# Kernel tuning notes

Hardware: AMD Instinct MI355X
Metric: run time of the kernel (lower is better)

## Reference

```python
import jax, jax.numpy as jnp
import numpy as np
import math

D = 768
H = 12
DK = D // H
DI = 3072
EPS_LN = 1e-12
NEG = -1e9


def layernorm(x, g, b):
    mu = jnp.mean(x, axis=-1, keepdims=True)
    var = jnp.mean(jnp.square(x - mu), axis=-1, keepdims=True)
    return (x - mu) * jax.lax.rsqrt(var + EPS_LN) * g + b


def setup_inputs() -> dict:
    key = jax.random.key(0)
    ks = jax.random.split(key, 16)
    B, S = 16, 512
    sd = 0.02
    inp = {
        "hidden_states": jax.random.normal(ks[0], (B, S, D), dtype=jnp.float32),
        "constituent_prior": jnp.zeros((B, S, S), dtype=jnp.float32),
        "attention_mask": jnp.ones((B, S), dtype=jnp.int32),
        # MultiHeadedAttention: 4 linears (q, k, v, out)
        "Wq": jax.random.normal(ks[1], (D, D)) * sd, "bq": jnp.zeros((D,)),
        "Wk": jax.random.normal(ks[2], (D, D)) * sd, "bk": jnp.zeros((D,)),
        "Wv": jax.random.normal(ks[3], (D, D)) * sd, "bv": jnp.zeros((D,)),
        "Wo": jax.random.normal(ks[4], (D, D)) * sd, "bo": jnp.zeros((D,)),
        # GroupAttention: key/query linears + LayerNorm
        "gWk": jax.random.normal(ks[5], (D, D)) * sd, "gbk": jnp.zeros((D,)),
        "gWq": jax.random.normal(ks[6], (D, D)) * sd, "gbq": jnp.zeros((D,)),
        "g_ln_g": jnp.ones((D,)), "g_ln_b": jnp.zeros((D,)),
        # BertIntermediate / BertOutput
        "Wi": jax.random.normal(ks[7], (D, DI)) * sd, "bi": jnp.zeros((DI,)),
        "Wout": jax.random.normal(ks[8], (DI, D)) * sd, "bout": jnp.zeros((D,)),
        "ln_g": jnp.ones((D,)), "ln_b": jnp.zeros((D,)),
    }
    return {k: v.astype(jnp.float32) if v.dtype == jnp.float32 or jnp.issubdtype(v.dtype, jnp.floating) else v for k, v in inp.items()}


def group_attention(x, attention_mask, prior, gWk, gbk, gWq, gbq, g_ln_g, g_ln_b):
    B, S, _ = x.shape
    a = jnp.eye(S, k=1, dtype=jnp.float32)      # super-diagonal
    c = jnp.eye(S, k=-1, dtype=jnp.float32)     # sub-diagonal
    eye = jnp.eye(S, dtype=jnp.float32)
    tri = jnp.triu(jnp.ones((S, S), dtype=jnp.float32))  # upper-tri incl. diag

    h = layernorm(x, g_ln_g, g_ln_b)
    k = h @ gWk + gbk
    q = h @ gWq + gbq
    scores = jnp.einsum("bsd,btd->bst", q, k) / D
    # mask[b,i,j] = attention_mask[b,j] & (a+c)[i,j]  (only +/-1 neighbors)
    mask = attention_mask.astype(jnp.float32)[:, None, :] * (a + c)[None]
    scores = jnp.where(mask == 0, NEG, scores)
    neigh = jax.nn.softmax(scores, axis=-1)
    neigh = jnp.sqrt(neigh * jnp.swapaxes(neigh, -2, -1) + 1e-9)
    neigh = prior + (1.0 - prior) * neigh

    # prefix log-sums along the super-diagonal via triangular matmuls
    t = jnp.where(a[None] == 0, 0.0, jnp.log(neigh + 1e-9)) @ tri
    C = jnp.exp(jnp.einsum("ij,bjk->bik", tri, t))
    C = jnp.where((tri - eye)[None] == 0, 0.0, C)   # keep strictly upper tri
    C = C + jnp.swapaxes(C, -2, -1) + jnp.where(eye[None] == 0, 1e-9, neigh)
    return C, neigh


def multi_head_attention(x, group_prob, attention_mask, Wq, bq, Wk, bk, Wv, bv, Wo, bo):
    B, S, _ = x.shape
    def split(y):  # [B,S,D] -> [B,H,S,DK]
        return y.reshape(B, S, H, DK).transpose(0, 2, 1, 3)
    q = split(x @ Wq + bq)
    k = split(x @ Wk + bk)
    v = split(x @ Wv + bv)
    scores = jnp.einsum("bhsd,bhtd->bhst", q, k) / math.sqrt(DK)
    eye = jnp.eye(S, dtype=jnp.int32)
    # combined mask: allow key j if attention_mask[b,j] or j == i (diagonal)
    cm = (attention_mask[:, None, None, :] | eye[None, None]) != 0
    scores = jnp.where(cm, scores, NEG)
    p = jax.nn.softmax(scores, axis=-1) * group_prob[:, None]  # [B,H,S,S]
    out = jnp.einsum("bhst,bhtd->bhsd", p, v)
    out = out.transpose(0, 2, 1, 3).reshape(B, S, D)
    return out @ Wo + bo


def reference(hidden_states, constituent_prior, attention_mask,
              Wq, bq, Wk, bk, Wv, bv, Wo, bo,
              gWk, gbk, gWq, gbq, g_ln_g, g_ln_b,
              Wi, bi, Wout, bout, ln_g, ln_b):
    C, neigh = group_attention(hidden_states, attention_mask, constituent_prior,
                               gWk, gbk, gWq, gbq, g_ln_g, g_ln_b)
    attn_out = multi_head_attention(hidden_states, C, attention_mask,
                                    Wq, bq, Wk, bk, Wv, bv, Wo, bo)
    inter = jax.nn.gelu(attn_out @ Wi + bi, approximate=False)
    layer_out = layernorm(inter @ Wout + bout + attn_out, ln_g, ln_b)
    return (layer_out, C, neigh, attn_out)
```

## Files before the change

### kernel.cpp

```cpp
#include <hip/hip_runtime.h>
#include <math.h>

typedef unsigned short ushort_t;
typedef __attribute__((ext_vector_type(8))) short bf16x8;
typedef __attribute__((ext_vector_type(4))) float f32x4;

#define Dt 768
#define Mrows 8192

__device__ __forceinline__ ushort_t f2b(float f) {
    union { float f; unsigned int u; } v; v.f = f;
    unsigned int u = v.u;
    unsigned int r = (u + 0x7fffu + ((u >> 16) & 1u)) >> 16;
    return (ushort_t)r;
}
__device__ __forceinline__ float b2f(ushort_t u) {
    union { unsigned int u; float f; } v; v.u = ((unsigned int)u) << 16;
    return v.f;
}
__device__ __forceinline__ f32x4 mfma16(bf16x8 a, bf16x8 b, f32x4 c) {
    return __builtin_amdgcn_mfma_f32_16x16x32_bf16(a, b, c, 0, 0, 0);
}
__device__ __forceinline__ float gelu_exact(float v) {
    return 0.5f * v * (1.0f + erff(v * 0.70710678118654752f));
}
__device__ __forceinline__ void gl2lds16(const ushort_t* g, ushort_t* l) {
    __builtin_amdgcn_global_load_lds((const __attribute__((address_space(1))) void*)g,
                                     (__attribute__((address_space(3))) void*)l,
                                     16, 0, 0);
}

__global__ __launch_bounds__(256)
void tconv6_kernel(const float* i0, const float* i1, const float* i2,
                   const float* i3, const float* i4, const float* i5,
                   ushort_t* o0, ushort_t* o1, ushort_t* o2,
                   ushort_t* o3, ushort_t* o4, ushort_t* o5)
{
    const float* in; ushort_t* out;
    switch (blockIdx.z) {
        case 0: in = i0; out = o0; break;
        case 1: in = i1; out = o1; break;
        case 2: in = i2; out = o2; break;
        case 3: in = i3; out = o3; break;
        case 4: in = i4; out = o4; break;
        default: in = i5; out = o5; break;
    }
    __shared__ float T[32][33];
    int t = threadIdx.x;
    int n0 = blockIdx.x * 32, k0 = blockIdx.y * 32;
    int r = t >> 3, c4 = (t & 7) * 4;
    float4 v = *(const float4*)(in + (size_t)(k0 + r) * 768 + n0 + c4);
    T[r][c4] = v.x; T[r][c4 + 1] = v.y; T[r][c4 + 2] = v.z; T[r][c4 + 3] = v.w;
    __syncthreads();
    int nl = t >> 3, k4 = (t & 7) * 4;
    unsigned int lo = (unsigned int)f2b(T[k4][nl]) | ((unsigned int)f2b(T[k4 + 1][nl]) << 16);
    unsigned int hi = (unsigned int)f2b(T[k4 + 2][nl]) | ((unsigned int)f2b(T[k4 + 3][nl]) << 16);
    uint2 o; o.x = lo; o.y = hi;
    *(uint2*)(out + (size_t)(n0 + nl) * 768 + k0 + k4) = o;
}

__global__ __launch_bounds__(256)
void tconv_kernel(const float* __restrict__ in, ushort_t* __restrict__ out,
                  int K, int N)
{
    __shared__ float T[32][33];
    int t = threadIdx.x;
    int n0 = blockIdx.x * 32, k0 = blockIdx.y * 32;
    int r = t >> 3, c4 = (t & 7) * 4;
    float4 v = *(const float4*)(in + (size_t)(k0 + r) * N + n0 + c4);
    T[r][c4] = v.x; T[r][c4 + 1] = v.y; T[r][c4 + 2] = v.z; T[r][c4 + 3] = v.w;
    __syncthreads();
    int nl = t >> 3, k4 = (t & 7) * 4;
    unsigned int lo = (unsigned int)f2b(T[k4][nl]) | ((unsigned int)f2b(T[k4 + 1][nl]) << 16);
    unsigned int hi = (unsigned int)f2b(T[k4 + 2][nl]) | ((unsigned int)f2b(T[k4 + 3][nl]) << 16);
    uint2 o; o.x = lo; o.y = hi;
    *(uint2*)(out + (size_t)(n0 + nl) * K + k0 + k4) = o;
}

__global__ __launch_bounds__(256)
void bconcat_kernel(const float* bq, const float* bk, const float* bv,
                    const float* gbq, const float* gbk,
                    float* bqkv, float* gbqk)
{
    int g = blockIdx.x * 256 + threadIdx.x;
    if (g < 768)       bqkv[g] = bq[g];
    else if (g < 1536) bqkv[g] = bk[g - 768];
    else if (g < 2304) bqkv[g] = bv[g - 1536];
    else if (g < 3072) gbqk[g - 2304] = gbq[g - 2304];
    else if (g < 3840) gbqk[g - 2304] = gbk[g - 3072];
}

__global__ __launch_bounds__(256)
void lnx_kernel(const float* __restrict__ x, const float* __restrict__ g,
                const float* __restrict__ be, ushort_t* __restrict__ xb,
                ushort_t* __restrict__ hb)
{
    int row = blockIdx.x;
    const float* xr = x + (size_t)row * Dt;
    int t = threadIdx.x;
    float v0 = xr[t], v1 = xr[t + 256], v2 = xr[t + 512];
    ushort_t* xrow = xb + (size_t)row * Dt;
    xrow[t] = f2b(v0); xrow[t + 256] = f2b(v1); xrow[t + 512] = f2b(v2);
    float s = v0 + v1 + v2;
    #pragma unroll
    for (int off = 32; off; off >>= 1) s += __shfl_xor(s, off, 64);
    __shared__ float r1[4], r2[4];
    if ((t & 63) == 0) r1[t >> 6] = s;
    __syncthreads();
    float mu = (r1[0] + r1[1] + r1[2] + r1[3]) * (1.0f / Dt);
    float d0 = v0 - mu, d1 = v1 - mu, d2 = v2 - mu;
    float sq = d0 * d0 + d1 * d1 + d2 * d2;
    #pragma unroll
    for (int off = 32; off; off >>= 1) sq += __shfl_xor(sq, off, 64);
    if ((t & 63) == 0) r2[t >> 6] = sq;
    __syncthreads();
    float var = (r2[0] + r2[1] + r2[2] + r2[3]) * (1.0f / Dt);
    float rs = 1.0f / sqrtf(var + 1e-12f);
    ushort_t* hrow = hb + (size_t)row * Dt;
    hrow[t]       = f2b(d0 * rs * g[t]       + be[t]);
    hrow[t + 256] = f2b(d1 * rs * g[t + 256] + be[t + 256]);
    hrow[t + 512] = f2b(d2 * rs * g[t + 512] + be[t + 512]);
}

__global__ __launch_bounds__(256)
void ln_kernel(const float* __restrict__ x, const float* __restrict__ g,
               const float* __restrict__ be, float* __restrict__ out)
{
    int row = blockIdx.x;
    const float* xr = x + (size_t)row * Dt;
    int t = threadIdx.x;
    float v0 = xr[t], v1 = xr[t + 256], v2 = xr[t + 512];
    float s = v0 + v1 + v2;
    #pragma unroll
    for (int off = 32; off; off >>= 1) s += __shfl_xor(s, off, 64);
    __shared__ float r1[4], r2[4];
    if ((t & 63) == 0) r1[t >> 6] = s;
    __syncthreads();
    float mu = (r1[0] + r1[1] + r1[2] + r1[3]) * (1.0f / Dt);
    float d0 = v0 - mu, d1 = v1 - mu, d2 = v2 - mu;
    float sq = d0 * d0 + d1 * d1 + d2 * d2;
    #pragma unroll
    for (int off = 32; off; off >>= 1) sq += __shfl_xor(sq, off, 64);
    if ((t & 63) == 0) r2[t >> 6] = sq;
    __syncthreads();
    float var = (r2[0] + r2[1] + r2[2] + r2[3]) * (1.0f / Dt);
    float rs = 1.0f / sqrtf(var + 1e-12f);
    float* orow = out + (size_t)row * Dt;
    orow[t]       = d0 * rs * g[t]       + be[t];
    orow[t + 256] = d1 * rs * g[t + 256] + be[t + 256];
    orow[t + 512] = d2 * rs * g[t + 512] + be[t + 512];
}

enum { EPI_BF16 = 1, EPI_QKV = 2, EPI_DUAL = 3, EPI_GELU = 4, EPI_RES = 5, EPI_ACC = 6 };

template<int BN, int EPI>
__global__ __launch_bounds__(256)
void gemm128(const ushort_t* __restrict__ A, const ushort_t* __restrict__ Bt,
             const float* __restrict__ bias, const float* __restrict__ res,
             float* __restrict__ Cf, ushort_t* __restrict__ O0,
             ushort_t* __restrict__ O1, ushort_t* __restrict__ O2,
             int K, int ldb, int ldc)
{
    constexpr int NF = BN / 32;
    constexpr int AHALF = 128 * 32;
    constexpr int BHALF = BN * 32;
    __shared__ ushort_t As[2 * AHALF];
    __shared__ ushort_t Bs[2 * BHALF];
    int t = threadIdx.x;
    int w = t >> 6, l = t & 63;
    int wr = w >> 1, wc = w & 1;
    int lr = l & 15, lg = l >> 4;

    int nwg = gridDim.x * gridDim.y;
    int bid = blockIdx.y * gridDim.x + blockIdx.x;
    int per = nwg >> 3;
    int sw  = (bid & 7) * per + (bid >> 3);
    int bn = (sw % gridDim.x) * BN;
    int bm = (sw / gridDim.x) * 128;

    const ushort_t* gA0 = A + (size_t)(bm + (t >> 2)) * K + ((t & 3) << 3);
    const ushort_t* gA1 = A + (size_t)(bm + 64 + (t >> 2)) * K + ((t & 3) << 3);
    const ushort_t* gB0 = Bt + (size_t)(bn + (t >> 2)) * ldb + ((t & 3) << 3);
    const ushort_t* gB1 = (BN == 128) ?
        Bt + (size_t)(bn + 64 + (t >> 2)) * ldb + ((t & 3) << 3) : nullptr;
    int woff = (w << 9);

    f32x4 acc[4][NF];
    #pragma unroll
    for (int m = 0; m < 4; ++m)
        #pragma unroll
        for (int n = 0; n < NF; ++n) acc[m][n] = (f32x4)0.0f;

    gl2lds16(gA0, As + woff);
    gl2lds16(gA1, As + 2048 + woff);
    gl2lds16(gB0, Bs + woff);
    if (BN == 128) gl2lds16(gB1, Bs + 2048 + woff);
    __syncthreads();

    int cur = 0;
    for (int k0 = 0; k0 < K; k0 += 32) {
        if (k0 + 32 < K) {
            int nb = (cur ^ 1);
            gl2lds16(gA0 + k0 + 32, As + nb * AHALF + woff);
            gl2lds16(gA1 + k0 + 32, As + nb * AHALF + 2048 + woff);
            gl2lds16(gB0 + k0 + 32, Bs + nb * BHALF + woff);
            if (BN == 128) gl2lds16(gB1 + k0 + 32, Bs + nb * BHALF + 2048 + woff);
        }
        const ushort_t* Ab = As + cur * AHALF;
        const ushort_t* Bb = Bs + cur * BHALF;
        bf16x8 af[4], bfv[NF];
        #pragma unroll
        for (int m = 0; m < 4; ++m)
            af[m] = *(const bf16x8*)&Ab[(wr * 64 + m * 16 + lr) * 32 + lg * 8];
        #pragma unroll
        for (int n = 0; n < NF; ++n)
            bfv[n] = *(const bf16x8*)&Bb[(wc * (BN / 2) + n * 16 + lr) * 32 + lg * 8];
        __builtin_amdgcn_s_setprio(1);
        #pragma unroll
        for (int m = 0; m < 4; ++m)
            #pragma unroll
            for (int n = 0; n < NF; ++n)
                acc[m][n] = mfma16(af[m], bfv[n], acc[m][n]);
        __builtin_amdgcn_s_setprio(0);
        __syncthreads();
        cur ^= 1;
    }

    #pragma unroll
    for (int m = 0; m < 4; ++m) {
        int row0 = bm + wr * 64 + m * 16 + lg * 4;
        #pragma unroll
        for (int n = 0; n < NF; ++n) {
            int ng = bn + wc * (BN / 2) + n * 16 + lr;
            float v0 = acc[m][n][0], v1 = acc[m][n][1];
            float v2 = acc[m][n][2], v3 = acc[m][n][3];
            if (EPI != EPI_ACC) {
                float bv = bias[ng];
                v0 += bv; v1 += bv; v2 += bv; v3 += bv;
            }
            if (EPI == EPI_BF16) {
                O0[(size_t)(row0 + 0) * ldc + ng] = f2b(v0);
                O0[(size_t)(row0 + 1) * ldc + ng] = f2b(v1);
                O0[(size_t)(row0 + 2) * ldc + ng] = f2b(v2);
                O0[(size_t)(row0 + 3) * ldc + ng] = f2b(v3);
            } else if (EPI == EPI_QKV) {
                if (bn < 768) {
                    O0[(size_t)(row0 + 0) * 768 + ng] = f2b(v0 * 0.125f);
                    O0[(size_t)(row0 + 1) * 768 + ng] = f2b(v1 * 0.125f);
                    O0[(size_t)(row0 + 2) * 768 + ng] = f2b(v2 * 0.125f);
                    O0[(size_t)(row0 + 3) * 768 + ng] = f2b(v3 * 0.125f);
                } else if (bn < 1536) {
                    int c = ng - 768;
                    O1[(size_t)(row0 + 0) * 768 + c] = f2b(v0);
                    O1[(size_t)(row0 + 1) * 768 + c] = f2b(v1);
                    O1[(size_t)(row0 + 2) * 768 + c] = f2b(v2);
                    O1[(size_t)(row0 + 3) * 768 + c] = f2b(v3);
                } else {
                    int dk = ng - 1536;
                    unsigned int lo = (unsigned int)f2b(v0) | ((unsigned int)f2b(v1) << 16);
                    unsigned int hi = (unsigned int)f2b(v2) | ((unsigned int)f2b(v3) << 16);
                    uint2 o; o.x = lo; o.y = hi;
                    *(uint2*)(O2 + (size_t)dk * Mrows + row0) = o;
                }
            } else if (EPI == EPI_DUAL) {
                Cf[(size_t)(row0 + 0) * ldc + ng] = v0;
                Cf[(size_t)(row0 + 1) * ldc + ng] = v1;
                Cf[(size_t)(row0 + 2) * ldc + ng] = v2;
                Cf[(size_t)(row0 + 3) * ldc + ng] = v3;
                O0[(size_t)(row0 + 0) * ldc + ng] = f2b(v0);
                O0[(size_t)(row0 + 1) * ldc + ng] = f2b(v1);
                O0[(size_t)(row0 + 2) * ldc + ng] = f2b(v2);
                O0[(size_t)(row0 + 3) * ldc + ng] = f2b(v3);
            } else if (EPI == EPI_GELU) {
                O0[(size_t)(row0 + 0) * ldc + ng] = f2b(gelu_exact(v0));
                O0[(size_t)(row0 + 1) * ldc + ng] = f2b(gelu_exact(v1));
                O0[(size_t)(row0 + 2) * ldc + ng] = f2b(gelu_exact(v2));
                O0[(size_t)(row0 + 3) * ldc + ng] = f2b(gelu_exact(v3));
            } else if (EPI == EPI_RES) {
                Cf[(size_t)(row0 + 0) * ldc + ng] = v0 + res[(size_t)(row0 + 0) * Dt + ng];
                Cf[(size_t)(row0 + 1) * ldc + ng] = v1 + res[(size_t)(row0 + 1) * Dt + ng];
                Cf[(size_t)(row0 + 2) * ldc + ng] = v2 + res[(size_t)(row0 + 2) * Dt + ng];
                Cf[(size_t)(row0 + 3) * ldc + ng] = v3 + res[(size_t)(row0 + 3) * Dt + ng];
            } else if (EPI == EPI_ACC) {
                Cf[(size_t)(row0 + 0) * ldc + ng] += v0;
                Cf[(size_t)(row0 + 1) * ldc + ng] += v1;
                Cf[(size_t)(row0 + 2) * ldc + ng] += v2;
                Cf[(size_t)(row0 + 3) * ldc + ng] += v3;
            }
        }
    }
}

__global__ __launch_bounds__(256)
void group_scores_kernel(const ushort_t* __restrict__ GQK, const int* __restrict__ am,
                         float* __restrict__ smU, float* __restrict__ smD,
                         int* __restrict__ emptyF)
{
    int gi = blockIdx.x;
    int b = gi >> 9, s = gi & 511;
    int t = threadIdx.x;
    const ushort_t* qr = GQK + (size_t)gi * 1536;
    bool hasU = (s < 511) && (am[(b << 9) + s + 1] != 0);
    bool hasD = (s > 0)   && (am[(b << 9) + s - 1] != 0);
    float su = 0.0f, sd = 0.0f;
    if (hasU) {
        const ushort_t* kr = GQK + (size_t)(gi + 1) * 1536 + 768;
        for (int c = t; c < Dt; c += 256) su += b2f(qr[c]) * b2f(kr[c]);
    }
    if (hasD) {
        const ushort_t* kr = GQK + (size_t)(gi - 1) * 1536 + 768;
        for (int c = t; c < Dt; c += 256) sd += b2f(qr[c]) * b2f(kr[c]);
    }
    #pragma unroll
    for (int off = 32; off; off >>= 1) { su += __shfl_xor(su, off, 64); sd += __shfl_xor(sd, off, 64); }
    __shared__ float rU[4], rD[4];
    if ((t & 63) == 0) { rU[t >> 6] = su; rD[t >> 6] = sd; }
    __syncthreads();
    if (t == 0) {
        su = (rU[0] + rU[1] + rU[2] + rU[3]) * (1.0f / Dt);
        sd = (rD[0] + rD[1] + rD[2] + rD[3]) * (1.0f / Dt);
        float u, d2; int emp = 0;
        if (hasU && hasD) {
            float m = fmaxf(su, sd);
            float eu = __expf(su - m), ed = __expf(sd - m);
            float inv = 1.0f / (eu + ed);
            u = eu * inv; d2 = ed * inv;
        } else if (hasU) { u = 1.0f; d2 = 0.0f; }
        else if (hasD)   { u = 0.0f; d2 = 1.0f; }
        else { u = d2 = 1.0f / 512.0f; emp = 1; }
        smU[gi] = u; smD[gi] = d2; emptyF[gi] = emp;
    }
}

__global__ __launch_bounds__(64)
void prefix_kernel(const float* __restrict__ prior, const float* __restrict__ smU,
                   const float* __restrict__ smD, float* __restrict__ P)
{
    int b = blockIdx.x;
    int l = threadIdx.x;
    float lv[8];
    float run = 0.0f;
    #pragma unroll
    for (int e = 0; e < 8; ++e) {
        int j = l * 8 + e;
        float lj = 0.0f;
        if (j < 511) {
            float pr = prior[((size_t)((b << 9) + j)) * 512 + j + 1];
            float nv = pr + (1.0f - pr) *
                       sqrtf(smU[(b << 9) + j] * smD[(b << 9) + j + 1] + 1e-9f);
            lj = logf(nv + 1e-9f);
        }
        lv[e] = run;
        run += lj;
    }
    float tot = run;
    float scan = tot;
    #pragma unroll
    for (int off = 1; off < 64; off <<= 1) {
        float n = __shfl_up(scan, off, 64);
        if (l >= off) scan += n;
    }
    float excl = scan - tot;
    #pragma unroll
    for (int e = 0; e < 8; ++e)
        P[b * 512 + l * 8 + e] = excl + lv[e];
}

__global__ __launch_bounds__(512)
void neigh_cfill_kernel(const float* __restrict__ prior,
                        const float* __restrict__ smU, const float* __restrict__ smD,
                        const int* __restrict__ emptyF, const float* __restrict__ P,
                        float* __restrict__ ne_out, float* __restrict__ C_out,
                        ushort_t* __restrict__ CB)
{
    int bi = blockIdx.x;
    int j  = threadIdx.x;
    int b = bi >> 9, i = bi & 511;
    int bj = (b << 9) + j;
    const float invS = 1.0f / 512.0f;
    float fij, fji;
    if (j == i + 1)      { fij = smU[bi]; fji = smD[bj]; }
    else if (j == i - 1) { fij = smD[bi]; fji = smU[bj]; }
    else { fij = emptyF[bi] ? invS : 0.0f; fji = emptyF[bj] ? invS : 0.0f; }
    float val = sqrtf(fij * fji + 1e-9f);
    float pr = prior[(size_t)bi * 512 + j];
    float nv = pr + (1.0f - pr) * val;
    ne_out[(size_t)bi * 512 + j] = nv;
    float pi = P[bi], pj = P[bj];
    float v;
    if (j > i)      v = expf(pj - pi) + 1e-9f;
    else if (j < i) v = expf(pi - pj) + 1e-9f;
    else            v = nv;
    C_out[(size_t)bi * 512 + j] = v;
    CB[(size_t)bi * 512 + j] = f2b(v);
}

#define SMAX 12.0f
__global__ __launch_bounds__(256)
void mha_mfma(const ushort_t* __restrict__ q, const ushort_t* __restrict__ k,
              const ushort_t* __restrict__ vt, const int* __restrict__ am,
              const ushort_t* __restrict__ CB, ushort_t* __restrict__ ctx)
{
    __shared__ ushort_t Qs[64][72];
    __shared__ ushort_t Ks[64][72];
    __shared__ ushort_t Vs[64][72];
    __shared__ ushort_t Ps[64][72];
    int t = threadIdx.x;
    int w = t >> 6, l = t & 63;
    int lr = l & 15, lg = l >> 4;
    int kb8 = lg << 3;
    int bid = (blockIdx.z * 12 + blockIdx.y) * 8 + blockIdx.x;
    int sw = (bid & 7) * 192 + (bid >> 3);
    int qt = sw & 7, h = (sw >> 3) % 12, b = sw / 96;
    int hoff = h * 64;
    int q0 = qt * 64;
    int q0g = (b << 9) + q0;
    int myrow = w * 16 + lg * 4;

    #pragma unroll
    for (int i = 0; i < 2; ++i) {
        int c = t + i * 256;
        int r = c >> 3, dc = (c & 7) << 3;
        *(uint4*)&Qs[r][dc] = *(const uint4*)(q + (size_t)(q0g + r) * Dt + hoff + dc);
    }

    f32x4 oacc[4];
    #pragma unroll
    for (int n = 0; n < 4; ++n) oacc[n] = (f32x4)0.0f;
    float l_run[4] = {0.0f, 0.0f, 0.0f, 0.0f};

    for (int kb = 0; kb < 8; ++kb) {
        __syncthreads();
        #pragma unroll
        for (int i = 0; i < 2; ++i) {
            int c = t + i * 256;
            int r = c >> 3, dc = (c & 7) << 3;
            *(uint4*)&Ks[r][dc] =
                *(const uint4*)(k + (size_t)((b << 9) + kb * 64 + r) * Dt + hoff + dc);
            *(uint4*)&Vs[r][dc] =
                *(const uint4*)(vt + (size_t)(hoff + r) * Mrows + (b << 9) + kb * 64 + dc);
        }
        __syncthreads();

        int amv[4];
        #pragma unroll
        for (int n = 0; n < 4; ++n) amv[n] = am[(b << 9) + kb * 64 + n * 16 + lr];
        float cc[4][4];
        #pragma unroll
        for (int n = 0; n < 4; ++n)
            #pragma unroll
            for (int r = 0; r < 4; ++r)
                cc[n][r] = b2f(CB[(size_t)(q0g + myrow + r) * 512 + kb * 64 + n * 16 + lr]);

        f32x4 s[4];
        #pragma unroll
        for (int n = 0; n < 4; ++n) s[n] = (f32x4)0.0f;
        __builtin_amdgcn_s_setprio(1);
        #pragma unroll
        for (int ks = 0; ks < 2; ++ks) {
            bf16x8 aq = *(const bf16x8*)&Qs[w * 16 + lr][ks * 32 + kb8];
            #pragma unroll
            for (int n = 0; n < 4; ++n) {
                bf16x8 bk = *(const bf16x8*)&Ks[n * 16 + lr][ks * 32 + kb8];
                s[n] = mfma16(aq, bk, s[n]);
            }
        }
        __builtin_amdgcn_s_setprio(0);

        float pf[4][4];
        #pragma unroll
        for (int n = 0; n < 4; ++n) {
            int key = kb * 64 + n * 16 + lr;
            #pragma unroll
            for (int r = 0; r < 4; ++r) {
                int qrow = q0 + myrow + r;
                bool ok = (amv[n] != 0) || (key == qrow);
                float p = ok ? __expf(s[n][r] - SMAX) : 0.0f;
                pf[n][r] = p;
                l_run[r] += p;
            }
        }
        #pragma unroll
        for (int n = 0; n < 4; ++n)
            #pragma unroll
            for (int r = 0; r < 4; ++r)
                Ps[myrow + r][n * 16 + lr] = f2b(pf[n][r] * cc[n][r]);

        __builtin_amdgcn_s_setprio(1);
        #pragma unroll
        for (int ks = 0; ks < 2; ++ks) {
            bf16x8 ap = *(const bf16x8*)&Ps[w * 16 + lr][ks * 32 + kb8];
            #pragma unroll
            for (int n = 0; n < 4; ++n) {
                bf16x8 bv = *(const bf16x8*)&Vs[n * 16 + lr][ks * 32 + kb8];
                oacc[n] = mfma16(ap, bv, oacc[n]);
            }
        }
        __builtin_amdgcn_s_setprio(0);
    }
    #pragma unroll
    for (int r = 0; r < 4; ++r) {
        #pragma unroll
        for (int off = 1; off < 16; off <<= 1)
            l_run[r] += __shfl_xor(l_run[r], off, 64);
    }
    #pragma unroll
    for (int r = 0; r < 4; ++r) {
        float inv = 1.0f / l_run[r];
        #pragma unroll
        for (int n = 0; n < 4; ++n)
            ctx[(size_t)(q0g + myrow + r) * Dt + hoff + n * 16 + lr] =
                f2b(oacc[n][r] * inv);
    }
}

extern "C" void kernel_launch(void* const* d_in, const int* in_sizes, int n_in,
                              void* d_out, int out_size, void* d_ws, size_t ws_size,
                              hipStream_t stream)
{
    (void)in_sizes; (void)n_in; (void)out_size; (void)ws_size;
    const float* x     = (const float*)d_in[0];
    const float* prior = (const float*)d_in[1];
    const int*   am    = (const int*)  d_in[2];
    const float* Wq = (const float*)d_in[3];   const float* bq = (const float*)d_in[4];
    const float* Wk = (const float*)d_in[5];   const float* bk = (const float*)d_in[6];
    const float* Wv = (const float*)d_in[7];   const float* bv = (const float*)d_in[8];
    const float* Wo = (const float*)d_in[9];   const float* bo = (const float*)d_in[10];
    const float* gWk = (const float*)d_in[11]; const float* gbk = (const float*)d_in[12];
    const float* gWq = (const float*)d_in[13]; const float* gbq = (const float*)d_in[14];
    const float* glng = (const float*)d_in[15]; const float* glnb = (const float*)d_in[16];
    const float* Wi = (const float*)d_in[17];  const float* bi = (const float*)d_in[18];
    const float* Wout = (const float*)d_in[19]; const float* bout = (const float*)d_in[20];
    const float* lng = (const float*)d_in[21]; const float* lnb = (const float*)d_in[22];

    float* out = (float*)d_out;
    float* o_layer = out;
    float* o_C     = out + (size_t)6291456;
    float* o_neigh = out + (size_t)10485760;
    float* o_attn  = out + (size_t)14680064;
    ushort_t* CB = (ushort_t*)o_attn;

    char* base = (char*)d_ws;
    ushort_t* WqkvT = (ushort_t*)(base);
    ushort_t* gWqkT = (ushort_t*)(base + 3538944);
    ushort_t* WoT   = (ushort_t*)(base + 5898240);
    ushort_t* WiT   = (ushort_t*)(base + 7077888);
    ushort_t* WoutT = (ushort_t*)(base + 11796480);
    float*    bqkv  = (float*)(base + 16515072);
    float*    gbqk  = (float*)(base + 16524288);
    float*    smU   = (float*)(base + 16530432);
    float*    smD   = (float*)(base + 16563200);
    float*    Ppre  = (float*)(base + 16595968);
    int*      emptyF= (int*)(base + 16628736);
    ushort_t* s0 = (ushort_t*)(base + 16661504);
    ushort_t* s1 = (ushort_t*)(base + 29244416);
    ushort_t* s2 = (ushort_t*)(base + 41827328);
    ushort_t* XB = s0;    ushort_t* CTXB = s0;
    ushort_t* HB = s1;    ushort_t* QB = s1;   ushort_t* AB16 = s1;
    ushort_t* GQK = s2;   ushort_t* KB = s2;   ushort_t* INTER = s2;
    ushort_t* VT = s2 + 6291456;

    tconv6_kernel<<<dim3(24, 24, 6), 256, 0, stream>>>(
        Wq, Wk, Wv, gWq, gWk, Wo,
        WqkvT, WqkvT + 589824, WqkvT + 1179648, gWqkT, gWqkT + 589824, WoT);
    tconv_kernel<<<dim3(96, 24), 256, 0, stream>>>(Wi, WiT, 768, 3072);
    tconv_kernel<<<dim3(24, 96), 256, 0, stream>>>(Wout, WoutT, 3072, 768);
    bconcat_kernel<<<15, 256, 0, stream>>>(bq, bk, bv, gbq, gbk, bqkv, gbqk);

    lnx_kernel<<<8192, 256, 0, stream>>>(x, glng, glnb, XB, HB);
    gemm128<128, EPI_BF16><<<dim3(12, 64), 256, 0, stream>>>(
        HB, gWqkT, gbqk, nullptr, nullptr, GQK, nullptr, nullptr, 768, 768, 1536);
    group_scores_kernel<<<8192, 256, 0, stream>>>(GQK, am, smU, smD, emptyF);
    prefix_kernel<<<16, 64, 0, stream>>>(prior, smU, smD, Ppre);
    neigh_cfill_kernel<<<8192, 512, 0, stream>>>(prior, smU, smD, emptyF, Ppre,
                                                 o_neigh, o_C, CB);

    gemm128<128, EPI_QKV><<<dim3(18, 64), 256, 0, stream>>>(
        XB, WqkvT, bqkv, nullptr, nullptr, QB, KB, VT, 768, 768, 768);
    mha_mfma<<<dim3(8, 12, 16), 256, 0, stream>>>(QB, KB, VT, am, CB, CTXB);
    gemm128<64, EPI_DUAL><<<dim3(12, 64), 256, 0, stream>>>(
        CTXB, WoT, bo, nullptr, o_attn, AB16, nullptr, nullptr, 768, 768, 768);

    for (int c = 0; c < 2; ++c) {
        gemm128<128, EPI_GELU><<<dim3(12, 64), 256, 0, stream>>>(
            AB16, WiT + (size_t)c * 1536 * 768, bi + (size_t)c * 1536, nullptr,
            nullptr, INTER, nullptr, nullptr, 768, 768, 1536);
        if (c == 0)
            gemm128<64, EPI_RES><<<dim3(12, 64), 256, 0, stream>>>(
                INTER, WoutT + (size_t)c * 1536, bout, o_attn, o_layer, nullptr,
                nullptr, nullptr, 1536, 3072, 768);
        else
            gemm128<64, EPI_ACC><<<dim3(12, 64), 256, 0, stream>>>(
                INTER, WoutT + (size_t)c * 1536, nullptr, nullptr, o_layer, nullptr,
                nullptr, nullptr, 1536, 3072, 768);
    }
    ln_kernel<<<8192, 256, 0, stream>>>(o_layer, lng, lnb, o_layer);
}
```

Baseline: 523.4 us.

## Triple-buffer GEMM LDS pipeline with XOR swizzle and unify 128x128 tiles

Reworks the bf16 MFMA GEMM to use a three-stage LDS ring with explicit vmcnt waits and raw barriers in place of double buffering plus __syncthreads. This lets two tiles of global loads stay in flight while the current one is computed. LDS rows are XOR-swizzled by 8-element chunk to cut bank conflicts on the fragment reads. The BN=64 variant is dropped, so the N=768 GEMMs now use 128-wide tiles with half as many workgroups, which costs occupancy and parallelism on those launches.

```diff
diff --git a/kernel.cpp b/kernel.cpp
--- a/kernel.cpp
+++ b/kernel.cpp
@@ -153,7 +153,7 @@
 
 enum { EPI_BF16 = 1, EPI_QKV = 2, EPI_DUAL = 3, EPI_GELU = 4, EPI_RES = 5, EPI_ACC = 6 };
 
-template<int BN, int EPI>
+template<int EPI>
 __global__ __launch_bounds__(256)
 void gemm128(const ushort_t* __restrict__ A, const ushort_t* __restrict__ Bt,
              const float* __restrict__ bias, const float* __restrict__ res,
@@ -161,11 +161,9 @@
              ushort_t* __restrict__ O1, ushort_t* __restrict__ O2,
              int K, int ldb, int ldc)
 {
-    constexpr int NF = BN / 32;
-    constexpr int AHALF = 128 * 32;
-    constexpr int BHALF = BN * 32;
-    __shared__ ushort_t As[2 * AHALF];
-    __shared__ ushort_t Bs[2 * BHALF];
+    constexpr int TSZ = 128 * 32;
+    __shared__ ushort_t As[3 * TSZ];
+    __shared__ ushort_t Bs[3 * TSZ];
     int t = threadIdx.x;
     int w = t >> 6, l = t & 63;
     int wr = w >> 1, wc = w & 1;
@@ -175,63 +173,78 @@
     int bid = blockIdx.y * gridDim.x + blockIdx.x;
     int per = nwg >> 3;
     int sw  = (bid & 7) * per + (bid >> 3);
-    int bn = (sw % gridDim.x) * BN;
+    int bn = (sw % gridDim.x) * 128;
     int bm = (sw / gridDim.x) * 128;
 
-    const ushort_t* gA0 = A + (size_t)(bm + (t >> 2)) * K + ((t & 3) << 3);
-    const ushort_t* gA1 = A + (size_t)(bm + 64 + (t >> 2)) * K + ((t & 3) << 3);
-    const ushort_t* gB0 = Bt + (size_t)(bn + (t >> 2)) * ldb + ((t & 3) << 3);
-    const ushort_t* gB1 = (BN == 128) ?
-        Bt + (size_t)(bn + 64 + (t >> 2)) * ldb + ((t & 3) << 3) : nullptr;
+    int srow = t >> 2;
+    int soct = (t & 3) ^ ((srow >> 1) & 3);
+    const ushort_t* gA0 = A + (size_t)(bm + srow) * K + (soct << 3);
+    const ushort_t* gA1 = A + (size_t)(bm + 64 + srow) * K + (soct << 3);
+    const ushort_t* gB0 = Bt + (size_t)(bn + srow) * ldb + (soct << 3);
+    const ushort_t* gB1 = Bt + (size_t)(bn + 64 + srow) * ldb + (soct << 3);
     int woff = (w << 9);
 
-    f32x4 acc[4][NF];
+    f32x4 acc[4][4];
     #pragma unroll
     for (int m = 0; m < 4; ++m)
         #pragma unroll
-        for (int n = 0; n < NF; ++n) acc[m][n] = (f32x4)0.0f;
-
+        for (int n = 0; n < 4; ++n) acc[m][n] = (f32x4)0.0f;
+
+    int nT = K >> 5;
     gl2lds16(gA0, As + woff);
     gl2lds16(gA1, As + 2048 + woff);
     gl2lds16(gB0, Bs + woff);
-    if (BN == 128) gl2lds16(gB1, Bs + 2048 + woff);
-    __syncthreads();
-
-    int cur = 0;
-    for (int k0 = 0; k0 < K; k0 += 32) {
-        if (k0 + 32 < K) {
-            int nb = (cur ^ 1);
-            gl2lds16(gA0 + k0 + 32, As + nb * AHALF + woff);
-            gl2lds16(gA1 + k0 + 32, As + nb * AHALF + 2048 + woff);
-            gl2lds16(gB0 + k0 + 32, Bs + nb * BHALF + woff);
-            if (BN == 128) gl2lds16(gB1 + k0 + 32, Bs + nb * BHALF + 2048 + woff);
-        }
-        const ushort_t* Ab = As + cur * AHALF;
-        const ushort_t* Bb = Bs + cur * BHALF;
-        bf16x8 af[4], bfv[NF];
-        #pragma unroll
-        for (int m = 0; m < 4; ++m)
-            af[m] = *(const bf16x8*)&Ab[(wr * 64 + m * 16 + lr) * 32 + lg * 8];
-        #pragma unroll
-        for (int n = 0; n < NF; ++n)
-            bfv[n] = *(const bf16x8*)&Bb[(wc * (BN / 2) + n * 16 + lr) * 32 + lg * 8];
+    gl2lds16(gB1, Bs + 2048 + woff);
+    gl2lds16(gA0 + 32, As + TSZ + woff);
+    gl2lds16(gA1 + 32, As + TSZ + 2048 + woff);
+    gl2lds16(gB0 + 32, Bs + TSZ + woff);
+    gl2lds16(gB1 + 32, Bs + TSZ + 2048 + woff);
+
+    int cb = 0, sb = 2;
+    for (int tt = 0; tt < nT; ++tt) {
+        if (tt + 2 < nT) {
+            int k0 = (tt + 2) << 5;
+            gl2lds16(gA0 + k0, As + sb * TSZ + woff);
+            gl2lds16(gA1 + k0, As + sb * TSZ + 2048 + woff);
+            gl2lds16(gB0 + k0, Bs + sb * TSZ + woff);
+            gl2lds16(gB1 + k0, Bs + sb * TSZ + 2048 + woff);
+        }
+        if (tt < nT - 2)       asm volatile("s_waitcnt vmcnt(8)" ::: "memory");
+        else if (tt == nT - 2) asm volatile("s_waitcnt vmcnt(4)" ::: "memory");
+        else                   asm volatile("s_waitcnt vmcnt(0)" ::: "memory");
+        __builtin_amdgcn_s_barrier();
+
+        const ushort_t* Ab = As + cb * TSZ;
+        const ushort_t* Bb = Bs + cb * TSZ;
+        bf16x8 af[4], bfv[4];
+        #pragma unroll
+        for (int m = 0; m < 4; ++m) {
+            int R = wr * 64 + m * 16 + lr;
+            af[m] = *(const bf16x8*)&Ab[R * 32 + ((lg ^ ((R >> 1) & 3)) << 3)];
+        }
+        #pragma unroll
+        for (int n = 0; n < 4; ++n) {
+            int R = wc * 64 + n * 16 + lr;
+            bfv[n] = *(const bf16x8*)&Bb[R * 32 + ((lg ^ ((R >> 1) & 3)) << 3)];
+        }
         __builtin_amdgcn_s_setprio(1);
         #pragma unroll
         for (int m = 0; m < 4; ++m)
             #pragma unroll
-            for (int n = 0; n < NF; ++n)
+            for (int n = 0; n < 4; ++n)
                 acc[m][n] = mfma16(af[m], bfv[n], acc[m][n]);
         __builtin_amdgcn_s_setprio(0);
-        __syncthreads();
-        cur ^= 1;
+        __builtin_amdgcn_s_barrier();
+        cb = (cb == 2) ? 0 : cb + 1;
+        sb = (sb == 2) ? 0 : sb + 1;
     }
 
     #pragma unroll
     for (int m = 0; m < 4; ++m) {
         int row0 = bm + wr * 64 + m * 16 + lg * 4;
         #pragma unroll
-        for (int n = 0; n < NF; ++n) {
-            int ng = bn + wc * (BN / 2) + n * 16 + lr;
+        for (int n = 0; n < 4; ++n) {
+            int ng = bn + wc * 64 + n * 16 + lr;
             float v0 = acc[m][n][0], v1 = acc[m][n][1];
             float v2 = acc[m][n][2], v3 = acc[m][n][3];
             if (EPI != EPI_ACC) {
@@ -568,29 +581,29 @@
     bconcat_kernel<<<15, 256, 0, stream>>>(bq, bk, bv, gbq, gbk, bqkv, gbqk);
 
     lnx_kernel<<<8192, 256, 0, stream>>>(x, glng, glnb, XB, HB);
-    gemm128<128, EPI_BF16><<<dim3(12, 64), 256, 0, stream>>>(
+    gemm128<EPI_BF16><<<dim3(12, 64), 256, 0, stream>>>(
         HB, gWqkT, gbqk, nullptr, nullptr, GQK, nullptr, nullptr, 768, 768, 1536);
     group_scores_kernel<<<8192, 256, 0, stream>>>(GQK, am, smU, smD, emptyF);
     prefix_kernel<<<16, 64, 0, stream>>>(prior, smU, smD, Ppre);
     neigh_cfill_kernel<<<8192, 512, 0, stream>>>(prior, smU, smD, emptyF, Ppre,
                                                  o_neigh, o_C, CB);
 
-    gemm128<128, EPI_QKV><<<dim3(18, 64), 256, 0, stream>>>(
+    gemm128<EPI_QKV><<<dim3(18, 64), 256, 0, stream>>>(
         XB, WqkvT, bqkv, nullptr, nullptr, QB, KB, VT, 768, 768, 768);
     mha_mfma<<<dim3(8, 12, 16), 256, 0, stream>>>(QB, KB, VT, am, CB, CTXB);
-    gemm128<64, EPI_DUAL><<<dim3(12, 64), 256, 0, stream>>>(
+    gemm128<EPI_DUAL><<<dim3(6, 64), 256, 0, stream>>>(
         CTXB, WoT, bo, nullptr, o_attn, AB16, nullptr, nullptr, 768, 768, 768);
 
     for (int c = 0; c < 2; ++c) {
-        gemm128<128, EPI_GELU><<<dim3(12, 64), 256, 0, stream>>>(
+        gemm128<EPI_GELU><<<dim3(12, 64), 256, 0, stream>>>(
             AB16, WiT + (size_t)c * 1536 * 768, bi + (size_t)c * 1536, nullptr,
             nullptr, INTER, nullptr, nullptr, 768, 768, 1536);
         if (c == 0)
-            gemm128<64, EPI_RES><<<dim3(12, 64), 256, 0, stream>>>(
+            gemm128<EPI_RES><<<dim3(6, 64), 256, 0, stream>>>(
                 INTER, WoutT + (size_t)c * 1536, bout, o_attn, o_layer, nullptr,
                 nullptr, nullptr, 1536, 3072, 768);
         else
-            gemm128<64, EPI_ACC><<<dim3(12, 64), 256, 0, stream>>>(
+            gemm128<EPI_ACC><<<dim3(6, 64), 256, 0, stream>>>(
                 INTER, WoutT + (size_t)c * 1536, nullptr, nullptr, o_layer, nullptr,
                 nullptr, nullptr, 1536, 3072, 768);
     }
```

New measurement: 562.6 us. 1.07x slower.
